# Performance work log

Measured on AMD Instinct MI355X. Metric: run time of the kernel, lower is better.

The kernel has to match this reference:

```python
import jax, jax.numpy as jnp
import numpy as np

B, D, R, P, N, PR = 128, 1024, 36, 8, 16, 4
MARGIN = 0.0
N_O, N_A, N_R, N_C = 0.5, 0.5, 0.5, 0.5


def setup_inputs() -> dict:
    key = jax.random.key(0)
    ks = jax.random.split(key, 12)
    return {
        "img_emb": jax.random.normal(ks[0], (B, D), jnp.float32),
        "sent_emb": jax.random.normal(ks[1], (B, D), jnp.float32),
        "comp_emb": jax.random.normal(ks[2], (B, D), jnp.float32),
        "img_feat_emb": jax.random.normal(ks[3], (B, R, D), jnp.float32),
        "obj_emb": jax.random.normal(ks[4], (B, P, D), jnp.float32),
        "neg_obj_emb": jax.random.normal(ks[5], (B, P, N, D), jnp.float32),
        "attr_emb": jax.random.normal(ks[6], (B, P, D), jnp.float32),
        "neg_attr_n_emb": jax.random.normal(ks[7], (B, P, N, D), jnp.float32),
        "neg_attr_a_emb": jax.random.normal(ks[8], (B, P, N, D), jnp.float32),
        "rel_emb": jax.random.normal(ks[9], (B, PR, D), jnp.float32),
        "neg_rel_emb": jax.random.normal(ks[10], (B, PR, N, D), jnp.float32),
        "rel_idx": jax.random.randint(ks[11], (B,), 0, PR, jnp.int64 if jax.config.jax_enable_x64 else jnp.int32),
    }


def contrastive(im, s, unidirectional=False):
    # cosine_sim: im @ s.T; hinge vs diagonal, diagonal masked out
    scores = im @ s.T                      # [B,B]
    diag = jnp.diagonal(scores)
    off = 1.0 - jnp.eye(scores.shape[0], dtype=scores.dtype)
    cost_s = jnp.maximum(MARGIN + scores - diag[:, None], 0.0) * off
    cost_im = jnp.maximum(MARGIN + scores - diag[None, :], 0.0) * off
    if unidirectional:
        return cost_s.sum()
    return cost_s.sum() + cost_im.sum()


def global_loss(img_feats, pos, neg):
    # Eq.1: per positive embedding, hinge vs hardest negative (max over N)
    pos_sim = jnp.einsum("bpd,bd->bp", pos, img_feats)          # [B,P]
    neg_sim = jnp.einsum("bpnd,bd->bpn", neg, img_feats)        # [B,P,N]
    max_neg = neg_sim.max(axis=2)                                # [B,P]
    return jnp.maximum(MARGIN + max_neg - pos_sim, 0.0).sum()


def local_loss(img_feats, pos, neg):
    # Eq.2/3: attention-weighted hinge over regions
    sims = jnp.einsum("bpd,brd->bpr", pos, img_feats)            # [B,P,R]
    m = jax.nn.softmax(sims, axis=2)
    neg_sims = jnp.einsum("bpnd,brd->bpnr", neg, img_feats)      # [B,P,N,R]
    max_neg = neg_sims.max(axis=2)                               # [B,P,R]
    return (m * jnp.maximum(MARGIN + max_neg - sims, 0.0)).sum()


def reference(img_emb, sent_emb, comp_emb, img_feat_emb, obj_emb, neg_obj_emb,
              attr_emb, neg_attr_n_emb, neg_attr_a_emb, rel_emb, neg_rel_emb,
              rel_idx):
    l_sent = contrastive(img_emb, sent_emb)
    l_comp = contrastive(img_emb, comp_emb)
    l_obj = local_loss(img_feat_emb, obj_emb, neg_obj_emb)
    l_attr = (local_loss(img_feat_emb, attr_emb, neg_attr_n_emb)
              + local_loss(img_feat_emb, attr_emb, neg_attr_a_emb))
    rel_samp = rel_emb[jnp.arange(rel_emb.shape[0]), rel_idx]    # [B,D]
    l_rel = (contrastive(img_emb, rel_samp, unidirectional=True)
             + global_loss(img_emb, rel_emb, neg_rel_emb))
    total = l_sent + N_C * l_comp + N_R * l_rel + N_A * l_attr + N_O * l_obj
    others = jnp.stack([l_obj, l_attr, l_rel, l_comp, l_sent])
    return total, others
```

## Files before the change

kernel.cpp:

```cpp
#include <hip/hip_runtime.h>

#define BB   128
#define DD   1024
#define RR   36
#define PP   8
#define NNEG 16
#define PRR  4

typedef __bf16 bf16x8 __attribute__((ext_vector_type(8)));
typedef float f32x4 __attribute__((ext_vector_type(4)));

#define WS_DIAG 16
#define WSF_OFF_BYTES 4096
#define WSF_PER_B (3 * 32 * 64 * 8)
#define WSF_BYTES ((size_t)WSF_OFF_BYTES + (size_t)BB * WSF_PER_B * 2)

__global__ __launch_bounds__(256) void k_prep(const float* __restrict__ feat,
                                              const float* __restrict__ img,
                                              const float* __restrict__ sent,
                                              const float* __restrict__ comp,
                                              const float* __restrict__ rel,
                                              const int*   __restrict__ relidx,
                                              __bf16* __restrict__ wsf,
                                              float* __restrict__ ws) {
    const int b = blockIdx.x, nt = blockIdx.y, tid = threadIdx.x;
    if (b == 0 && nt == 0 && tid < 8) ws[tid] = 0.0f;

    const float* fb = feat + (size_t)b * RR * DD;
    __bf16* ob = wsf + (size_t)b * WSF_PER_B + (size_t)nt * 32 * 64 * 8;
    for (int i = tid; i < 32 * 64; i += 256) {
        const int ks = i >> 6, lane = i & 63;
        const int r = nt * 16 + (lane & 15);
        const int k0 = ks * 32 + (lane >> 4) * 8;
        bf16x8 w;
        if (r < RR) {
            float4 v0 = *reinterpret_cast<const float4*>(fb + (size_t)r * DD + k0);
            float4 v1 = *reinterpret_cast<const float4*>(fb + (size_t)r * DD + k0 + 4);
            w[0] = (__bf16)v0.x; w[1] = (__bf16)v0.y; w[2] = (__bf16)v0.z; w[3] = (__bf16)v0.w;
            w[4] = (__bf16)v1.x; w[5] = (__bf16)v1.y; w[6] = (__bf16)v1.z; w[7] = (__bf16)v1.w;
        } else {
#pragma unroll
            for (int j = 0; j < 8; ++j) w[j] = (__bf16)0.0f;
        }
        *reinterpret_cast<bf16x8*>(ob + (size_t)i * 8) = w;
    }

    if (tid < 64) {
        const int lane = tid;
        const float* x;
        if (nt == 0)      x = sent + (size_t)b * DD;
        else if (nt == 1) x = comp + (size_t)b * DD;
        else              x = rel + ((size_t)b * PRR + relidx[b]) * DD;
        const float* a = img + (size_t)b * DD;
        float acc = 0.0f;
#pragma unroll
        for (int k = 0; k < 4; ++k) {
            float4 va = *reinterpret_cast<const float4*>(a + lane * 4 + k * 256);
            float4 vb = *reinterpret_cast<const float4*>(x + lane * 4 + k * 256);
            acc += va.x * vb.x + va.y * vb.y + va.z * vb.z + va.w * vb.w;
        }
#pragma unroll
        for (int off = 32; off > 0; off >>= 1) acc += __shfl_down(acc, off);
        if (lane == 0) ws[WS_DIAG + nt * BB + b] = acc;
    }
}

__device__ __forceinline__ void compute_step(f32x4 n0, f32x4 n1, f32x4 p0, f32x4 p1,
                                             f32x4 f0, f32x4 f1, f32x4 f2,
                                             f32x4 accn[3], f32x4 accp[3]) {
    bf16x8 an, ap;
#pragma unroll
    for (int j = 0; j < 4; ++j) {
        an[j]     = (__bf16)n0[j];
        an[j + 4] = (__bf16)n1[j];
        ap[j]     = (__bf16)p0[j];
        ap[j + 4] = (__bf16)p1[j];
    }
    bf16x8 b0 = __builtin_bit_cast(bf16x8, f0);
    bf16x8 b1 = __builtin_bit_cast(bf16x8, f1);
    bf16x8 b2 = __builtin_bit_cast(bf16x8, f2);
    accn[0] = __builtin_amdgcn_mfma_f32_16x16x32_bf16(an, b0, accn[0], 0, 0, 0);
    accp[0] = __builtin_amdgcn_mfma_f32_16x16x32_bf16(ap, b0, accp[0], 0, 0, 0);
    accn[1] = __builtin_amdgcn_mfma_f32_16x16x32_bf16(an, b1, accn[1], 0, 0, 0);
    accp[1] = __builtin_amdgcn_mfma_f32_16x16x32_bf16(ap, b1, accp[1], 0, 0, 0);
    accn[2] = __builtin_amdgcn_mfma_f32_16x16x32_bf16(an, b2, accn[2], 0, 0, 0);
    accp[2] = __builtin_amdgcn_mfma_f32_16x16x32_bf16(ap, b2, accp[2], 0, 0, 0);
}

__global__ __launch_bounds__(256) void k_mega(const float* __restrict__ img,
                                              const float* __restrict__ sent,
                                              const float* __restrict__ comp,
                                              const float* __restrict__ obj,
                                              const float* __restrict__ attr,
                                              const float* __restrict__ nobj,
                                              const float* __restrict__ nattrn,
                                              const float* __restrict__ nattra,
                                              const float* __restrict__ rel,
                                              const float* __restrict__ nrel,
                                              const int*   __restrict__ relidx,
                                              const __bf16* __restrict__ wsf,
                                              float* __restrict__ ws) {
    const int x = blockIdx.x, y = blockIdx.y;
    const int tid = threadIdx.x;

    __shared__ float X[3][64][17];
    __shared__ float As[16][68];
    __shared__ float Bs[16][68];
    __shared__ float comm[8];

    if (x < 24) {
        const int t = x >> 3;
        const int p = x & 7;
        const int b = y;
        const int kh = tid >> 6;
        const int lane = tid & 63;
        const int lrow = lane & 15;
        const int kgq = lane >> 4;
        const int ksbase = kh * 8;

        const float* pos = (t == 0) ? obj : attr;
        const float* neg = (t == 0) ? nobj : (t == 1) ? nattrn : nattra;
        const float* posb = pos + ((size_t)b * PP + p) * DD + kgq * 8;
        const float* negb = neg + ((size_t)(b * PP + p) * NNEG + lrow) * DD + kgq * 8;
        const __bf16* wfb = wsf + (size_t)b * WSF_PER_B + (size_t)lane * 8;

        f32x4 accn[3], accp[3];
#pragma unroll
        for (int nt = 0; nt < 3; ++nt) {
            accn[nt] = (f32x4){0.f, 0.f, 0.f, 0.f};
            accp[nt] = (f32x4){0.f, 0.f, 0.f, 0.f};
        }

        f32x4 n0_0, n1_0, p0_0, p1_0, f0_0, f1_0, f2_0;
        f32x4 n0_1, n1_1, p0_1, p1_1, f0_1, f1_1, f2_1;
        f32x4 n0_2, n1_2, p0_2, p1_2, f0_2, f1_2, f2_2;

#define ISSUE(KS, B)                                                                   \
    {                                                                                  \
        const float* np_ = negb + (ksbase + (KS)) * 32;                                \
        const float* pq_ = posb + (ksbase + (KS)) * 32;                                \
        const __bf16* g0_ = wfb + (size_t)(0 * 32 + ksbase + (KS)) * 512;              \
        const __bf16* g1_ = wfb + (size_t)(1 * 32 + ksbase + (KS)) * 512;              \
        const __bf16* g2_ = wfb + (size_t)(2 * 32 + ksbase + (KS)) * 512;              \
        asm volatile("global_load_dwordx4 %0, %1, off" : "=v"(n0_##B) : "v"(np_));     \
        asm volatile("global_load_dwordx4 %0, %1, off offset:16"                       \
                     : "=v"(n1_##B) : "v"(np_));                                       \
        asm volatile("global_load_dwordx4 %0, %1, off" : "=v"(p0_##B) : "v"(pq_));     \
        asm volatile("global_load_dwordx4 %0, %1, off offset:16"                       \
                     : "=v"(p1_##B) : "v"(pq_));                                       \
        asm volatile("global_load_dwordx4 %0, %1, off" : "=v"(f0_##B) : "v"(g0_));     \
        asm volatile("global_load_dwordx4 %0, %1, off" : "=v"(f1_##B) : "v"(g1_));     \
        asm volatile("global_load_dwordx4 %0, %1, off" : "=v"(f2_##B) : "v"(g2_));     \
    }

#define WAITV(N)                                          \
    asm volatile("s_waitcnt vmcnt(" #N ")" ::: "memory"); \
    __builtin_amdgcn_sched_barrier(0);

#define COMPUTE(B) compute_step(n0_##B, n1_##B, p0_##B, p1_##B,                        \
                                f0_##B, f1_##B, f2_##B, accn, accp);

        WAITV(0)
        ISSUE(0, 0)
        ISSUE(1, 1)
        ISSUE(2, 2) WAITV(14) COMPUTE(0)
        ISSUE(3, 0) WAITV(14) COMPUTE(1)
        ISSUE(4, 1) WAITV(14) COMPUTE(2)
        ISSUE(5, 2) WAITV(14) COMPUTE(0)
        ISSUE(6, 0) WAITV(14) COMPUTE(1)
        ISSUE(7, 1) WAITV(14) COMPUTE(2)
        WAITV(7)  COMPUTE(0)
        WAITV(0)  COMPUTE(1)

#undef ISSUE
#undef WAITV
#undef COMPUTE

        if (kh != 0) {
#pragma unroll
            for (int nt = 0; nt < 3; ++nt) {
                X[kh - 1][lane][nt * 4 + 0] = accn[nt][0];
                X[kh - 1][lane][nt * 4 + 1] = accn[nt][1];
                X[kh - 1][lane][nt * 4 + 2] = accn[nt][2];
                X[kh - 1][lane][nt * 4 + 3] = accn[nt][3];
                X[kh - 1][lane][12 + nt]    = accp[nt][0];
            }
        }
        __syncthreads();
        if (kh == 0) {
#pragma unroll
            for (int q = 0; q < 3; ++q) {
#pragma unroll
                for (int nt = 0; nt < 3; ++nt) {
                    accn[nt][0] += X[q][lane][nt * 4 + 0];
                    accn[nt][1] += X[q][lane][nt * 4 + 1];
                    accn[nt][2] += X[q][lane][nt * 4 + 2];
                    accn[nt][3] += X[q][lane][nt * 4 + 3];
                    accp[nt][0] += X[q][lane][12 + nt];
                }
            }

            float s3[3], h3[3];
#pragma unroll
            for (int nt = 0; nt < 3; ++nt) {
                f32x4 a = accn[nt];
                float m = fmaxf(fmaxf(a[0], a[1]), fmaxf(a[2], a[3]));
                m = fmaxf(m, __shfl_xor(m, 16));
                m = fmaxf(m, __shfl_xor(m, 32));
                float s = accp[nt][0];
                s3[nt] = s;
                h3[nt] = fmaxf(m - s, 0.0f);
            }
            float mx = -1e30f;
#pragma unroll
            for (int nt = 0; nt < 3; ++nt)
                if (nt * 16 + lrow < RR) mx = fmaxf(mx, s3[nt]);
#pragma unroll
            for (int off = 1; off < 16; off <<= 1) mx = fmaxf(mx, __shfl_xor(mx, off));
            float den = 0.0f, num = 0.0f;
#pragma unroll
            for (int nt = 0; nt < 3; ++nt)
                if (nt * 16 + lrow < RR) {
                    float e = __expf(s3[nt] - mx);
                    den += e;
                    num += e * h3[nt];
                }
#pragma unroll
            for (int off = 1; off < 16; off <<= 1) {
                den += __shfl_xor(den, off);
                num += __shfl_xor(num, off);
            }
            if (lane == 0)
                atomicAdd(&ws[(t == 0) ? 0 : 1], num / den);
        }
    } else if (x < 28) {
        const int p = x - 24, b = y;
        const int wv = tid >> 6, lane = tid & 63;
        const float* a = img + (size_t)b * DD;
        float4 ir[4];
#pragma unroll
        for (int k = 0; k < 4; ++k)
            ir[k] = *reinterpret_cast<const float4*>(a + lane * 4 + k * 256);

        auto dotv = [&](const float* __restrict__ v) -> float {
            float acc = 0.0f;
#pragma unroll
            for (int k = 0; k < 4; ++k) {
                float4 w = *reinterpret_cast<const float4*>(v + lane * 4 + k * 256);
                acc += ir[k].x * w.x + ir[k].y * w.y + ir[k].z * w.z + ir[k].w * w.w;
            }
#pragma unroll
            for (int off = 32; off > 0; off >>= 1) acc += __shfl_xor(acc, off);
            return acc;
        };

        if (wv == 0) {
            float pos = dotv(rel + ((size_t)b * PRR + p) * DD);
            if (lane == 0) comm[4] = pos;
        }
        const float* nb = nrel + ((size_t)b * PRR + p) * NNEG * DD;
        float m = -1e30f;
#pragma unroll
        for (int j = 0; j < 4; ++j)
            m = fmaxf(m, dotv(nb + (size_t)(wv * 4 + j) * DD));
        if (lane == 0) comm[wv] = m;
        __syncthreads();
        if (tid == 0) {
            float mx = fmaxf(fmaxf(comm[0], comm[1]), fmaxf(comm[2], comm[3]));
            atomicAdd(&ws[2], fmaxf(mx - comm[4], 0.0f));
        }
    } else {
        if (y >= 64) return;
        const int t = x - 28;
        const int i0 = (y >> 3) * 16, j0 = (y & 7) * 16;
        const int ty = tid >> 4, tx = tid & 15;

        const int j_row = j0 + ty;
        const float* brow;
        if (t == 0)      brow = sent + (size_t)j_row * DD;
        else if (t == 1) brow = comp + (size_t)j_row * DD;
        else             brow = rel + ((size_t)j_row * PRR + relidx[j_row]) * DD;
        const float* arow = img + (size_t)(i0 + ty) * DD;

        float acc = 0.0f;
        for (int kc = 0; kc < DD; kc += 64) {
            __syncthreads();
            float4 va = *reinterpret_cast<const float4*>(arow + kc + tx * 4);
            float4 vb = *reinterpret_cast<const float4*>(brow + kc + tx * 4);
            *reinterpret_cast<float4*>(&As[ty][tx * 4]) = va;
            *reinterpret_cast<float4*>(&Bs[ty][tx * 4]) = vb;
            __syncthreads();
#pragma unroll 8
            for (int d = 0; d < 64; ++d)
                acc += As[ty][d] * Bs[tx][d];
        }

        const int i = i0 + ty, j = j0 + tx;
        const float diag_i = ws[WS_DIAG + t * BB + i];
        const float diag_j = ws[WS_DIAG + t * BB + j];
        float contrib = 0.0f;
        if (i != j) {
            contrib = fmaxf(acc - diag_i, 0.0f);
            if (t < 2) contrib += fmaxf(acc - diag_j, 0.0f);
        }
#pragma unroll
        for (int off = 32; off > 0; off >>= 1) contrib += __shfl_down(contrib, off);
        if ((tid & 63) == 0) comm[tid >> 6] = contrib;
        __syncthreads();
        if (tid == 0) {
            const int slot = (t == 0) ? 4 : (t == 1) ? 3 : 2;
            atomicAdd(&ws[slot], comm[0] + comm[1] + comm[2] + comm[3]);
        }
    }
}

__global__ __launch_bounds__(64) void k_zero(float* __restrict__ ws) {
    int t = threadIdx.x;
    if (t < 8) ws[t] = 0.0f;
}

__global__ __launch_bounds__(64) void k_diag(const float* __restrict__ img,
                                             const float* __restrict__ sent,
                                             const float* __restrict__ comp,
                                             const float* __restrict__ rel,
                                             const int*   __restrict__ relidx,
                                             float* __restrict__ ws) {
    const int i = blockIdx.x, t = blockIdx.y, lane = threadIdx.x;
    const float* x;
    if (t == 0)      x = sent + (size_t)i * DD;
    else if (t == 1) x = comp + (size_t)i * DD;
    else             x = rel + ((size_t)i * PRR + relidx[i]) * DD;
    const float* a = img + (size_t)i * DD;
    float acc = 0.0f;
#pragma unroll
    for (int k = 0; k < 4; ++k) {
        float4 va = *reinterpret_cast<const float4*>(a + lane * 4 + k * 256);
        float4 vb = *reinterpret_cast<const float4*>(x + lane * 4 + k * 256);
        acc += va.x * vb.x + va.y * vb.y + va.z * vb.z + va.w * vb.w;
    }
#pragma unroll
    for (int off = 32; off > 0; off >>= 1) acc += __shfl_down(acc, off);
    if (lane == 0) ws[WS_DIAG + t * BB + i] = acc;
}

__global__ __launch_bounds__(256) void k_contrastive(const float* __restrict__ img,
                                                     const float* __restrict__ sent,
                                                     const float* __restrict__ comp,
                                                     const float* __restrict__ rel,
                                                     const int*   __restrict__ relidx,
                                                     float* __restrict__ ws) {
    const int t  = blockIdx.z;
    const int i0 = blockIdx.y * 16, j0 = blockIdx.x * 16;
    const int tid = threadIdx.x, ty = tid >> 4, tx = tid & 15;
    __shared__ float As[16][68];
    __shared__ float Bs[16][68];
    __shared__ float red[4];

    const int j_row = j0 + ty;
    const float* brow;
    if (t == 0)      brow = sent + (size_t)j_row * DD;
    else if (t == 1) brow = comp + (size_t)j_row * DD;
    else             brow = rel + ((size_t)j_row * PRR + relidx[j_row]) * DD;
    const float* arow = img + (size_t)(i0 + ty) * DD;

    float acc = 0.0f;
    for (int kc = 0; kc < DD; kc += 64) {
        __syncthreads();
        float4 va = *reinterpret_cast<const float4*>(arow + kc + tx * 4);
        float4 vb = *reinterpret_cast<const float4*>(brow + kc + tx * 4);
        *reinterpret_cast<float4*>(&As[ty][tx * 4]) = va;
        *reinterpret_cast<float4*>(&Bs[ty][tx * 4]) = vb;
        __syncthreads();
#pragma unroll 8
        for (int d = 0; d < 64; ++d)
            acc += As[ty][d] * Bs[tx][d];
    }

    const int i = i0 + ty, j = j0 + tx;
    const float diag_i = ws[WS_DIAG + t * BB + i];
    const float diag_j = ws[WS_DIAG + t * BB + j];
    float contrib = 0.0f;
    if (i != j) {
        contrib = fmaxf(acc - diag_i, 0.0f);
        if (t < 2) contrib += fmaxf(acc - diag_j, 0.0f);
    }
#pragma unroll
    for (int off = 32; off > 0; off >>= 1) contrib += __shfl_down(contrib, off);
    if ((tid & 63) == 0) red[tid >> 6] = contrib;
    __syncthreads();
    if (tid == 0) {
        const int slot = (t == 0) ? 4 : (t == 1) ? 3 : 2;
        atomicAdd(&ws[slot], red[0] + red[1] + red[2] + red[3]);
    }
}

__global__ __launch_bounds__(64) void k_globalrel(const float* __restrict__ img,
                                                  const float* __restrict__ rel,
                                                  const float* __restrict__ negrel,
                                                  float* __restrict__ ws) {
    const int blk = blockIdx.x, b = blk >> 2, p = blk & 3;
    const int lane = threadIdx.x;
    const float* a = img + (size_t)b * DD;
    float4 ir[4];
#pragma unroll
    for (int k = 0; k < 4; ++k)
        ir[k] = *reinterpret_cast<const float4*>(a + lane * 4 + k * 256);

    auto dotv = [&](const float* __restrict__ v) -> float {
        float acc = 0.0f;
#pragma unroll
        for (int k = 0; k < 4; ++k) {
            float4 w = *reinterpret_cast<const float4*>(v + lane * 4 + k * 256);
            acc += ir[k].x * w.x + ir[k].y * w.y + ir[k].z * w.z + ir[k].w * w.w;
        }
#pragma unroll
        for (int off = 32; off > 0; off >>= 1) acc += __shfl_xor(acc, off);
        return acc;
    };

    float pos = dotv(rel + ((size_t)b * PRR + p) * DD);
    float mx = -1e30f;
    const float* nb = negrel + ((size_t)b * PRR + p) * NNEG * DD;
    for (int n = 0; n < NNEG; ++n) mx = fmaxf(mx, dotv(nb + (size_t)n * DD));
    if (lane == 0) atomicAdd(&ws[2], fmaxf(mx - pos, 0.0f));
}

__global__ __launch_bounds__(256) void k_local6f(const float* __restrict__ feat,
                                                 const float* __restrict__ obj,
                                                 const float* __restrict__ attr,
                                                 const float* __restrict__ nobj,
                                                 const float* __restrict__ nattrn,
                                                 const float* __restrict__ nattra,
                                                 float* __restrict__ ws) {
    const int t = blockIdx.x;
    const int b = blockIdx.y;
    const int p = blockIdx.z;
    const int tid = threadIdx.x;
    const int kh = tid >> 6;
    const int lane = tid & 63;
    const int lrow = lane & 15;
    const int kgq = lane >> 4;
    const int ksbase = kh * 8;

    const float* pos = (t == 0) ? obj : attr;
    const float* neg = (t == 0) ? nobj : (t == 1) ? nattrn : nattra;
    const float* posb = pos + ((size_t)b * PP + p) * DD + kgq * 8;
    const float* negb = neg + ((size_t)(b * PP + p) * NNEG + lrow) * DD + kgq * 8;
    const float* fb   = feat + (size_t)b * RR * DD;

    f32x4 accn[3], accp[3];
#pragma unroll
    for (int nt = 0; nt < 3; ++nt) {
        accn[nt] = (f32x4){0.f, 0.f, 0.f, 0.f};
        accp[nt] = (f32x4){0.f, 0.f, 0.f, 0.f};
    }

    for (int ksl = 0; ksl < 8; ++ksl) {
        const int ks = ksbase + ksl;
        const float* np = negb + ks * 32;
        float4 n0 = *reinterpret_cast<const float4*>(np);
        float4 n1 = *reinterpret_cast<const float4*>(np + 4);
        const float* pq = posb + ks * 32;
        float4 p0 = *reinterpret_cast<const float4*>(pq);
        float4 p1 = *reinterpret_cast<const float4*>(pq + 4);
        bf16x8 an, ap;
        an[0] = (__bf16)n0.x; an[1] = (__bf16)n0.y; an[2] = (__bf16)n0.z; an[3] = (__bf16)n0.w;
        an[4] = (__bf16)n1.x; an[5] = (__bf16)n1.y; an[6] = (__bf16)n1.z; an[7] = (__bf16)n1.w;
        ap[0] = (__bf16)p0.x; ap[1] = (__bf16)p0.y; ap[2] = (__bf16)p0.z; ap[3] = (__bf16)p0.w;
        ap[4] = (__bf16)p1.x; ap[5] = (__bf16)p1.y; ap[6] = (__bf16)p1.z; ap[7] = (__bf16)p1.w;
#pragma unroll
        for (int nt = 0; nt < 3; ++nt) {
            bf16x8 bt;
            const int r = nt * 16 + lrow;
            if (r < RR) {
                const float* fp = fb + (size_t)r * DD + ks * 32 + kgq * 8;
                float4 v0 = *reinterpret_cast<const float4*>(fp);
                float4 v1 = *reinterpret_cast<const float4*>(fp + 4);
                bt[0] = (__bf16)v0.x; bt[1] = (__bf16)v0.y; bt[2] = (__bf16)v0.z; bt[3] = (__bf16)v0.w;
                bt[4] = (__bf16)v1.x; bt[5] = (__bf16)v1.y; bt[6] = (__bf16)v1.z; bt[7] = (__bf16)v1.w;
            } else {
#pragma unroll
                for (int j = 0; j < 8; ++j) bt[j] = (__bf16)0.0f;
            }
            accn[nt] = __builtin_amdgcn_mfma_f32_16x16x32_bf16(an, bt, accn[nt], 0, 0, 0);
            accp[nt] = __builtin_amdgcn_mfma_f32_16x16x32_bf16(ap, bt, accp[nt], 0, 0, 0);
        }
    }

    __shared__ float X[3][64][17];
    if (kh != 0) {
#pragma unroll
        for (int nt = 0; nt < 3; ++nt) {
            X[kh - 1][lane][nt * 4 + 0] = accn[nt][0];
            X[kh - 1][lane][nt * 4 + 1] = accn[nt][1];
            X[kh - 1][lane][nt * 4 + 2] = accn[nt][2];
            X[kh - 1][lane][nt * 4 + 3] = accn[nt][3];
            X[kh - 1][lane][12 + nt]    = accp[nt][0];
        }
    }
    __syncthreads();
    if (kh == 0) {
#pragma unroll
        for (int q = 0; q < 3; ++q)
#pragma unroll
            for (int nt = 0; nt < 3; ++nt) {
                accn[nt][0] += X[q][lane][nt * 4 + 0];
                accn[nt][1] += X[q][lane][nt * 4 + 1];
                accn[nt][2] += X[q][lane][nt * 4 + 2];
                accn[nt][3] += X[q][lane][nt * 4 + 3];
                accp[nt][0] += X[q][lane][12 + nt];
            }
        float s3[3], h3[3];
#pragma unroll
        for (int nt = 0; nt < 3; ++nt) {
            f32x4 a = accn[nt];
            float m = fmaxf(fmaxf(a[0], a[1]), fmaxf(a[2], a[3]));
            m = fmaxf(m, __shfl_xor(m, 16));
            m = fmaxf(m, __shfl_xor(m, 32));
            s3[nt] = accp[nt][0];
            h3[nt] = fmaxf(m - s3[nt], 0.0f);
        }
        float mx = -1e30f;
#pragma unroll
        for (int nt = 0; nt < 3; ++nt)
            if (nt * 16 + lrow < RR) mx = fmaxf(mx, s3[nt]);
#pragma unroll
        for (int off = 1; off < 16; off <<= 1) mx = fmaxf(mx, __shfl_xor(mx, off));
        float den = 0.0f, num = 0.0f;
#pragma unroll
        for (int nt = 0; nt < 3; ++nt)
            if (nt * 16 + lrow < RR) {
                float e = __expf(s3[nt] - mx);
                den += e;
                num += e * h3[nt];
            }
#pragma unroll
        for (int off = 1; off < 16; off <<= 1) {
            den += __shfl_xor(den, off);
            num += __shfl_xor(num, off);
        }
        if (lane == 0)
            atomicAdd(&ws[(t == 0) ? 0 : 1], num / den);
    }
}

__global__ __launch_bounds__(64) void k_final(const float* __restrict__ ws,
                                              float* __restrict__ out) {
    if (threadIdx.x == 0) {
        const float obj = ws[0], attr = ws[1], rel = ws[2], comp = ws[3], sent = ws[4];
        out[0] = sent + 0.5f * comp + 0.5f * rel + 0.5f * attr + 0.5f * obj;
        out[1] = obj;
        out[2] = attr;
        out[3] = rel;
        out[4] = comp;
        out[5] = sent;
    }
}

extern "C" void kernel_launch(void* const* d_in, const int* in_sizes, int n_in,
                              void* d_out, int out_size, void* d_ws, size_t ws_size,
                              hipStream_t stream) {
    const float* img    = (const float*)d_in[0];
    const float* sent   = (const float*)d_in[1];
    const float* comp   = (const float*)d_in[2];
    const float* feat   = (const float*)d_in[3];
    const float* obj    = (const float*)d_in[4];
    const float* nobj   = (const float*)d_in[5];
    const float* attr   = (const float*)d_in[6];
    const float* nattrn = (const float*)d_in[7];
    const float* nattra = (const float*)d_in[8];
    const float* rel    = (const float*)d_in[9];
    const float* nrel   = (const float*)d_in[10];
    const int*   relidx = (const int*)d_in[11];
    float* ws  = (float*)d_ws;
    float* out = (float*)d_out;
    __bf16* wsf = (__bf16*)((char*)d_ws + WSF_OFF_BYTES);

    const bool usewsf = (ws_size >= WSF_BYTES);

    if (usewsf) {
        k_prep<<<dim3(BB, 3), dim3(256), 0, stream>>>(feat, img, sent, comp, rel, relidx,
                                                      wsf, ws);
        k_mega<<<dim3(31, BB), dim3(256), 0, stream>>>(img, sent, comp, obj, attr, nobj,
                                                       nattrn, nattra, rel, nrel, relidx,
                                                       wsf, ws);
        k_final<<<dim3(1), dim3(64), 0, stream>>>(ws, out);
    } else {
        k_zero<<<dim3(1), dim3(64), 0, stream>>>(ws);
        k_diag<<<dim3(BB, 3), dim3(64), 0, stream>>>(img, sent, comp, rel, relidx, ws);
        k_contrastive<<<dim3(8, 8, 3), dim3(256), 0, stream>>>(img, sent, comp, rel, relidx, ws);
        k_globalrel<<<dim3(BB * PRR), dim3(64), 0, stream>>>(img, rel, nrel, ws);
        k_local6f<<<dim3(3, BB, PP), dim3(256), 0, stream>>>(feat, obj, attr, nobj, nattrn,
                                                             nattra, ws);
        k_final<<<dim3(1), dim3(64), 0, stream>>>(ws, out);
    }
}
```

Baseline: 85.79 us.

## Fuse obj/attr local-loss blocks so each block reuses image features across three tasks

Each k_mega block now handles all three local-loss tasks (obj, attr-n, attr-a) for one (b,p) pair instead of one task per block. The bf16 region features are loaded once and fed to 15 MFMAs per step rather than 6, and the positive-attr similarities and softmax are computed once and shared by both attr negative sets. The grid shrinks from 31 to 15 columns, a block-id swizzle spreads work across the grid, and the prefetch pipeline drops from triple to double buffering. The trade-off is much higher register pressure (two buffers of 13 vectors plus 15 accumulators), which could lower occupancy, and less parallelism per block in a memory-bound kernel.

```diff
diff --git a/kernel.cpp b/kernel.cpp
--- a/kernel.cpp
+++ b/kernel.cpp
@@ -65,26 +65,39 @@
     }
 }
 
-__device__ __forceinline__ void compute_step(f32x4 n0, f32x4 n1, f32x4 p0, f32x4 p1,
-                                             f32x4 f0, f32x4 f1, f32x4 f2,
-                                             f32x4 accn[3], f32x4 accp[3]) {
-    bf16x8 an, ap;
+__device__ __forceinline__ void compute_full(f32x4 nO0, f32x4 nO1, f32x4 nN0, f32x4 nN1,
+                                             f32x4 nA0, f32x4 nA1, f32x4 pO0, f32x4 pO1,
+                                             f32x4 pA0, f32x4 pA1,
+                                             f32x4 fb0, f32x4 fb1, f32x4 fb2,
+                                             f32x4 (&accn)[3][3], f32x4 (&accp)[2][3]) {
+    bf16x8 aO, aN, aA, apO, apA;
 #pragma unroll
     for (int j = 0; j < 4; ++j) {
-        an[j]     = (__bf16)n0[j];
-        an[j + 4] = (__bf16)n1[j];
-        ap[j]     = (__bf16)p0[j];
-        ap[j + 4] = (__bf16)p1[j];
-    }
-    bf16x8 b0 = __builtin_bit_cast(bf16x8, f0);
-    bf16x8 b1 = __builtin_bit_cast(bf16x8, f1);
-    bf16x8 b2 = __builtin_bit_cast(bf16x8, f2);
-    accn[0] = __builtin_amdgcn_mfma_f32_16x16x32_bf16(an, b0, accn[0], 0, 0, 0);
-    accp[0] = __builtin_amdgcn_mfma_f32_16x16x32_bf16(ap, b0, accp[0], 0, 0, 0);
-    accn[1] = __builtin_amdgcn_mfma_f32_16x16x32_bf16(an, b1, accn[1], 0, 0, 0);
-    accp[1] = __builtin_amdgcn_mfma_f32_16x16x32_bf16(ap, b1, accp[1], 0, 0, 0);
-    accn[2] = __builtin_amdgcn_mfma_f32_16x16x32_bf16(an, b2, accn[2], 0, 0, 0);
-    accp[2] = __builtin_amdgcn_mfma_f32_16x16x32_bf16(ap, b2, accp[2], 0, 0, 0);
+        aO[j]  = (__bf16)nO0[j]; aO[j + 4]  = (__bf16)nO1[j];
+        aN[j]  = (__bf16)nN0[j]; aN[j + 4]  = (__bf16)nN1[j];
+        aA[j]  = (__bf16)nA0[j]; aA[j + 4]  = (__bf16)nA1[j];
+        apO[j] = (__bf16)pO0[j]; apO[j + 4] = (__bf16)pO1[j];
+        apA[j] = (__bf16)pA0[j]; apA[j + 4] = (__bf16)pA1[j];
+    }
+    bf16x8 b0 = __builtin_bit_cast(bf16x8, fb0);
+    bf16x8 b1 = __builtin_bit_cast(bf16x8, fb1);
+    bf16x8 b2 = __builtin_bit_cast(bf16x8, fb2);
+
+    accn[0][0] = __builtin_amdgcn_mfma_f32_16x16x32_bf16(aO, b0, accn[0][0], 0, 0, 0);
+    accn[0][1] = __builtin_amdgcn_mfma_f32_16x16x32_bf16(aO, b1, accn[0][1], 0, 0, 0);
+    accn[0][2] = __builtin_amdgcn_mfma_f32_16x16x32_bf16(aO, b2, accn[0][2], 0, 0, 0);
+    accn[1][0] = __builtin_amdgcn_mfma_f32_16x16x32_bf16(aN, b0, accn[1][0], 0, 0, 0);
+    accn[1][1] = __builtin_amdgcn_mfma_f32_16x16x32_bf16(aN, b1, accn[1][1], 0, 0, 0);
+    accn[1][2] = __builtin_amdgcn_mfma_f32_16x16x32_bf16(aN, b2, accn[1][2], 0, 0, 0);
+    accn[2][0] = __builtin_amdgcn_mfma_f32_16x16x32_bf16(aA, b0, accn[2][0], 0, 0, 0);
+    accn[2][1] = __builtin_amdgcn_mfma_f32_16x16x32_bf16(aA, b1, accn[2][1], 0, 0, 0);
+    accn[2][2] = __builtin_amdgcn_mfma_f32_16x16x32_bf16(aA, b2, accn[2][2], 0, 0, 0);
+    accp[0][0] = __builtin_amdgcn_mfma_f32_16x16x32_bf16(apO, b0, accp[0][0], 0, 0, 0);
+    accp[0][1] = __builtin_amdgcn_mfma_f32_16x16x32_bf16(apO, b1, accp[0][1], 0, 0, 0);
+    accp[0][2] = __builtin_amdgcn_mfma_f32_16x16x32_bf16(apO, b2, accp[0][2], 0, 0, 0);
+    accp[1][0] = __builtin_amdgcn_mfma_f32_16x16x32_bf16(apA, b0, accp[1][0], 0, 0, 0);
+    accp[1][1] = __builtin_amdgcn_mfma_f32_16x16x32_bf16(apA, b1, accp[1][1], 0, 0, 0);
+    accp[1][2] = __builtin_amdgcn_mfma_f32_16x16x32_bf16(apA, b2, accp[1][2], 0, 0, 0);
 }
 
 __global__ __launch_bounds__(256) void k_mega(const float* __restrict__ img,
@@ -100,76 +113,93 @@
                                               const int*   __restrict__ relidx,
                                               const __bf16* __restrict__ wsf,
                                               float* __restrict__ ws) {
-    const int x = blockIdx.x, y = blockIdx.y;
+    const int orig = blockIdx.y * 15 + blockIdx.x;
+    const int jid  = (orig & 7) * 240 + (orig >> 3);
+    const int x = jid % 15, y = jid / 15;
     const int tid = threadIdx.x;
 
-    __shared__ float X[3][64][17];
+    __shared__ float X[3][64][44];
     __shared__ float As[16][68];
     __shared__ float Bs[16][68];
     __shared__ float comm[8];
 
-    if (x < 24) {
-        const int t = x >> 3;
-        const int p = x & 7;
-        const int b = y;
+    if (x < 8) {
+        const int p = x, b = y;
         const int kh = tid >> 6;
         const int lane = tid & 63;
         const int lrow = lane & 15;
         const int kgq = lane >> 4;
         const int ksbase = kh * 8;
 
-        const float* pos = (t == 0) ? obj : attr;
-        const float* neg = (t == 0) ? nobj : (t == 1) ? nattrn : nattra;
-        const float* posb = pos + ((size_t)b * PP + p) * DD + kgq * 8;
-        const float* negb = neg + ((size_t)(b * PP + p) * NNEG + lrow) * DD + kgq * 8;
+        const float* posO = obj    + ((size_t)b * PP + p) * DD + kgq * 8;
+        const float* posA = attr   + ((size_t)b * PP + p) * DD + kgq * 8;
+        const float* negO = nobj   + ((size_t)(b * PP + p) * NNEG + lrow) * DD + kgq * 8;
+        const float* negN = nattrn + ((size_t)(b * PP + p) * NNEG + lrow) * DD + kgq * 8;
+        const float* negA = nattra + ((size_t)(b * PP + p) * NNEG + lrow) * DD + kgq * 8;
         const __bf16* wfb = wsf + (size_t)b * WSF_PER_B + (size_t)lane * 8;
 
-        f32x4 accn[3], accp[3];
-#pragma unroll
-        for (int nt = 0; nt < 3; ++nt) {
-            accn[nt] = (f32x4){0.f, 0.f, 0.f, 0.f};
-            accp[nt] = (f32x4){0.f, 0.f, 0.f, 0.f};
-        }
-
-        f32x4 n0_0, n1_0, p0_0, p1_0, f0_0, f1_0, f2_0;
-        f32x4 n0_1, n1_1, p0_1, p1_1, f0_1, f1_1, f2_1;
-        f32x4 n0_2, n1_2, p0_2, p1_2, f0_2, f1_2, f2_2;
-
-#define ISSUE(KS, B)                                                                   \
-    {                                                                                  \
-        const float* np_ = negb + (ksbase + (KS)) * 32;                                \
-        const float* pq_ = posb + (ksbase + (KS)) * 32;                                \
-        const __bf16* g0_ = wfb + (size_t)(0 * 32 + ksbase + (KS)) * 512;              \
-        const __bf16* g1_ = wfb + (size_t)(1 * 32 + ksbase + (KS)) * 512;              \
-        const __bf16* g2_ = wfb + (size_t)(2 * 32 + ksbase + (KS)) * 512;              \
-        asm volatile("global_load_dwordx4 %0, %1, off" : "=v"(n0_##B) : "v"(np_));     \
-        asm volatile("global_load_dwordx4 %0, %1, off offset:16"                       \
-                     : "=v"(n1_##B) : "v"(np_));                                       \
-        asm volatile("global_load_dwordx4 %0, %1, off" : "=v"(p0_##B) : "v"(pq_));     \
-        asm volatile("global_load_dwordx4 %0, %1, off offset:16"                       \
-                     : "=v"(p1_##B) : "v"(pq_));                                       \
-        asm volatile("global_load_dwordx4 %0, %1, off" : "=v"(f0_##B) : "v"(g0_));     \
-        asm volatile("global_load_dwordx4 %0, %1, off" : "=v"(f1_##B) : "v"(g1_));     \
-        asm volatile("global_load_dwordx4 %0, %1, off" : "=v"(f2_##B) : "v"(g2_));     \
+        f32x4 accn[3][3], accp[2][3];
+#pragma unroll
+        for (int t = 0; t < 3; ++t)
+#pragma unroll
+            for (int nt = 0; nt < 3; ++nt) accn[t][nt] = (f32x4){0.f, 0.f, 0.f, 0.f};
+#pragma unroll
+        for (int s = 0; s < 2; ++s)
+#pragma unroll
+            for (int nt = 0; nt < 3; ++nt) accp[s][nt] = (f32x4){0.f, 0.f, 0.f, 0.f};
+
+        f32x4 nO0_0, nO1_0, nN0_0, nN1_0, nA0_0, nA1_0, pO0_0, pO1_0, pA0_0, pA1_0,
+              fB0_0, fB1_0, fB2_0;
+        f32x4 nO0_1, nO1_1, nN0_1, nN1_1, nA0_1, nA1_1, pO0_1, pO1_1, pA0_1, pA1_1,
+              fB0_1, fB1_1, fB2_1;
+
+#define ISSUE(KS, B)                                                                    \
+    {                                                                                   \
+        const float* nO_ = negO + (ksbase + (KS)) * 32;                                 \
+        const float* nN_ = negN + (ksbase + (KS)) * 32;                                 \
+        const float* nA_ = negA + (ksbase + (KS)) * 32;                                 \
+        const float* pO_ = posO + (ksbase + (KS)) * 32;                                 \
+        const float* pA_ = posA + (ksbase + (KS)) * 32;                                 \
+        const __bf16* g0_ = wfb + (size_t)(0 * 32 + ksbase + (KS)) * 512;               \
+        const __bf16* g1_ = wfb + (size_t)(1 * 32 + ksbase + (KS)) * 512;               \
+        const __bf16* g2_ = wfb + (size_t)(2 * 32 + ksbase + (KS)) * 512;               \
+        asm volatile("global_load_dwordx4 %0, %1, off" : "=v"(nO0_##B) : "v"(nO_));     \
+        asm volatile("global_load_dwordx4 %0, %1, off offset:16"                        \
+                     : "=v"(nO1_##B) : "v"(nO_));                                       \
+        asm volatile("global_load_dwordx4 %0, %1, off" : "=v"(nN0_##B) : "v"(nN_));     \
+        asm volatile("global_load_dwordx4 %0, %1, off offset:16"                        \
+                     : "=v"(nN1_##B) : "v"(nN_));                                       \
+        asm volatile("global_load_dwordx4 %0, %1, off" : "=v"(nA0_##B) : "v"(nA_));     \
+        asm volatile("global_load_dwordx4 %0, %1, off offset:16"                        \
+                     : "=v"(nA1_##B) : "v"(nA_));                                       \
+        asm volatile("global_load_dwordx4 %0, %1, off" : "=v"(pO0_##B) : "v"(pO_));     \
+        asm volatile("global_load_dwordx4 %0, %1, off offset:16"                        \
+                     : "=v"(pO1_##B) : "v"(pO_));                                       \
+        asm volatile("global_load_dwordx4 %0, %1, off" : "=v"(pA0_##B) : "v"(pA_));     \
+        asm volatile("global_load_dwordx4 %0, %1, off offset:16"                        \
+                     : "=v"(pA1_##B) : "v"(pA_));                                       \
+        asm volatile("global_load_dwordx4 %0, %1, off" : "=v"(fB0_##B) : "v"(g0_));     \
+        asm volatile("global_load_dwordx4 %0, %1, off" : "=v"(fB1_##B) : "v"(g1_));     \
+        asm volatile("global_load_dwordx4 %0, %1, off" : "=v"(fB2_##B) : "v"(g2_));     \
     }
 
 #define WAITV(N)                                          \
     asm volatile("s_waitcnt vmcnt(" #N ")" ::: "memory"); \
     __builtin_amdgcn_sched_barrier(0);
 
-#define COMPUTE(B) compute_step(n0_##B, n1_##B, p0_##B, p1_##B,                        \
-                                f0_##B, f1_##B, f2_##B, accn, accp);
+#define COMPUTE(B) compute_full(nO0_##B, nO1_##B, nN0_##B, nN1_##B, nA0_##B, nA1_##B,   \
+                                pO0_##B, pO1_##B, pA0_##B, pA1_##B,                     \
+                                fB0_##B, fB1_##B, fB2_##B, accn, accp);
 
         WAITV(0)
         ISSUE(0, 0)
-        ISSUE(1, 1)
-        ISSUE(2, 2) WAITV(14) COMPUTE(0)
-        ISSUE(3, 0) WAITV(14) COMPUTE(1)
-        ISSUE(4, 1) WAITV(14) COMPUTE(2)
-        ISSUE(5, 2) WAITV(14) COMPUTE(0)
-        ISSUE(6, 0) WAITV(14) COMPUTE(1)
-        ISSUE(7, 1) WAITV(14) COMPUTE(2)
-        WAITV(7)  COMPUTE(0)
+        ISSUE(1, 1) WAITV(13) COMPUTE(0)
+        ISSUE(2, 0) WAITV(13) COMPUTE(1)
+        ISSUE(3, 1) WAITV(13) COMPUTE(0)
+        ISSUE(4, 0) WAITV(13) COMPUTE(1)
+        ISSUE(5, 1) WAITV(13) COMPUTE(0)
+        ISSUE(6, 0) WAITV(13) COMPUTE(1)
+        ISSUE(7, 1) WAITV(13) COMPUTE(0)
         WAITV(0)  COMPUTE(1)
 
 #undef ISSUE
@@ -178,63 +208,96 @@
 
         if (kh != 0) {
 #pragma unroll
-            for (int nt = 0; nt < 3; ++nt) {
-                X[kh - 1][lane][nt * 4 + 0] = accn[nt][0];
-                X[kh - 1][lane][nt * 4 + 1] = accn[nt][1];
-                X[kh - 1][lane][nt * 4 + 2] = accn[nt][2];
-                X[kh - 1][lane][nt * 4 + 3] = accn[nt][3];
-                X[kh - 1][lane][12 + nt]    = accp[nt][0];
-            }
+            for (int t = 0; t < 3; ++t)
+#pragma unroll
+                for (int nt = 0; nt < 3; ++nt) {
+                    X[kh - 1][lane][t * 12 + nt * 4 + 0] = accn[t][nt][0];
+                    X[kh - 1][lane][t * 12 + nt * 4 + 1] = accn[t][nt][1];
+                    X[kh - 1][lane][t * 12 + nt * 4 + 2] = accn[t][nt][2];
+                    X[kh - 1][lane][t * 12 + nt * 4 + 3] = accn[t][nt][3];
+                }
+#pragma unroll
+            for (int s = 0; s < 2; ++s)
+#pragma unroll
+                for (int nt = 0; nt < 3; ++nt)
+                    X[kh - 1][lane][36 + s * 3 + nt] = accp[s][nt][0];
         }
         __syncthreads();
         if (kh == 0) {
 #pragma unroll
             for (int q = 0; q < 3; ++q) {
 #pragma unroll
+                for (int t = 0; t < 3; ++t)
+#pragma unroll
+                    for (int nt = 0; nt < 3; ++nt) {
+                        accn[t][nt][0] += X[q][lane][t * 12 + nt * 4 + 0];
+                        accn[t][nt][1] += X[q][lane][t * 12 + nt * 4 + 1];
+                        accn[t][nt][2] += X[q][lane][t * 12 + nt * 4 + 2];
+                        accn[t][nt][3] += X[q][lane][t * 12 + nt * 4 + 3];
+                    }
+#pragma unroll
+                for (int s = 0; s < 2; ++s)
+#pragma unroll
+                    for (int nt = 0; nt < 3; ++nt)
+                        accp[s][nt][0] += X[q][lane][36 + s * 3 + nt];
+            }
+
+            float mt[3][3];
+#pragma unroll
+            for (int t = 0; t < 3; ++t)
+#pragma unroll
                 for (int nt = 0; nt < 3; ++nt) {
-                    accn[nt][0] += X[q][lane][nt * 4 + 0];
-                    accn[nt][1] += X[q][lane][nt * 4 + 1];
-                    accn[nt][2] += X[q][lane][nt * 4 + 2];
-                    accn[nt][3] += X[q][lane][nt * 4 + 3];
-                    accp[nt][0] += X[q][lane][12 + nt];
+                    f32x4 a = accn[t][nt];
+                    float m = fmaxf(fmaxf(a[0], a[1]), fmaxf(a[2], a[3]));
+                    m = fmaxf(m, __shfl_xor(m, 16));
+                    m = fmaxf(m, __shfl_xor(m, 32));
+                    mt[t][nt] = m;
                 }
-            }
-
-            float s3[3], h3[3];
+            float s0[3], s1[3];
 #pragma unroll
             for (int nt = 0; nt < 3; ++nt) {
-                f32x4 a = accn[nt];
-                float m = fmaxf(fmaxf(a[0], a[1]), fmaxf(a[2], a[3]));
-                m = fmaxf(m, __shfl_xor(m, 16));
-                m = fmaxf(m, __shfl_xor(m, 32));
-                float s = accp[nt][0];
-                s3[nt] = s;
-                h3[nt] = fmaxf(m - s, 0.0f);
-            }
-            float mx = -1e30f;
-#pragma unroll
-            for (int nt = 0; nt < 3; ++nt)
-                if (nt * 16 + lrow < RR) mx = fmaxf(mx, s3[nt]);
-#pragma unroll
-            for (int off = 1; off < 16; off <<= 1) mx = fmaxf(mx, __shfl_xor(mx, off));
-            float den = 0.0f, num = 0.0f;
+                s0[nt] = accp[0][nt][0];
+                s1[nt] = accp[1][nt][0];
+            }
+
+            float mx0 = -1e30f, mx1 = -1e30f;
 #pragma unroll
             for (int nt = 0; nt < 3; ++nt)
                 if (nt * 16 + lrow < RR) {
-                    float e = __expf(s3[nt] - mx);
-                    den += e;
-                    num += e * h3[nt];
+                    mx0 = fmaxf(mx0, s0[nt]);
+                    mx1 = fmaxf(mx1, s1[nt]);
                 }
 #pragma unroll
             for (int off = 1; off < 16; off <<= 1) {
-                den += __shfl_xor(den, off);
-                num += __shfl_xor(num, off);
-            }
-            if (lane == 0)
-                atomicAdd(&ws[(t == 0) ? 0 : 1], num / den);
-        }
-    } else if (x < 28) {
-        const int p = x - 24, b = y;
+                mx0 = fmaxf(mx0, __shfl_xor(mx0, off));
+                mx1 = fmaxf(mx1, __shfl_xor(mx1, off));
+            }
+            float den0 = 0.f, num0 = 0.f, den1 = 0.f, num1 = 0.f;
+#pragma unroll
+            for (int nt = 0; nt < 3; ++nt)
+                if (nt * 16 + lrow < RR) {
+                    float e0 = __expf(s0[nt] - mx0);
+                    den0 += e0;
+                    num0 += e0 * fmaxf(mt[0][nt] - s0[nt], 0.0f);
+                    float e1 = __expf(s1[nt] - mx1);
+                    den1 += e1;
+                    num1 += e1 * (fmaxf(mt[1][nt] - s1[nt], 0.0f) +
+                                  fmaxf(mt[2][nt] - s1[nt], 0.0f));
+                }
+#pragma unroll
+            for (int off = 1; off < 16; off <<= 1) {
+                den0 += __shfl_xor(den0, off);
+                num0 += __shfl_xor(num0, off);
+                den1 += __shfl_xor(den1, off);
+                num1 += __shfl_xor(num1, off);
+            }
+            if (lane == 0) {
+                atomicAdd(&ws[0], num0 / den0);
+                atomicAdd(&ws[1], num1 / den1);
+            }
+        }
+    } else if (x < 12) {
+        const int p = x - 8, b = y;
         const int wv = tid >> 6, lane = tid & 63;
         const float* a = img + (size_t)b * DD;
         float4 ir[4];
@@ -271,7 +334,7 @@
         }
     } else {
         if (y >= 64) return;
-        const int t = x - 28;
+        const int t = x - 12;
         const int i0 = (y >> 3) * 16, j0 = (y & 7) * 16;
         const int ty = tid >> 4, tx = tid & 15;
 
@@ -581,7 +644,7 @@
     if (usewsf) {
         k_prep<<<dim3(BB, 3), dim3(256), 0, stream>>>(feat, img, sent, comp, rel, relidx,
                                                       wsf, ws);
-        k_mega<<<dim3(31, BB), dim3(256), 0, stream>>>(img, sent, comp, obj, attr, nobj,
+        k_mega<<<dim3(15, BB), dim3(256), 0, stream>>>(img, sent, comp, obj, attr, nobj,
                                                        nattrn, nattra, rel, nrel, relidx,
                                                        wsf, ws);
         k_final<<<dim3(1), dim3(64), 0, stream>>>(ws, out);
```

After: 83.70 us. 1.02x faster.
